# Kernel tuning notes

Measured on AMD Instinct MI355X. Metric: run time of the kernel, lower is better.

## Reference

```python
import jax, jax.numpy as jnp
import numpy as np

N = 5000      # nodes
E = 80000     # edges (avg degree 16)
B = 8         # batch of graph signals sharing one graph
IN = 30       # input feature dim (10 steps x 3)
H = 4         # attention heads
D = 64        # hidden dim per head
HD = H * D    # 256
OUT = 3       # output features per step
NUM_GAT_LAYERS = 4  # num_layer=5 -> 1 + (5-2) layers
EPS = 1e-5


def setup_inputs() -> dict:
    key = jax.random.key(0)
    ks = jax.random.split(key, 40)
    inp = {}
    inp["xx"] = jax.random.normal(ks[0], (B, N, IN), dtype=jnp.float32)
    inp["src"] = jax.random.randint(ks[1], (E,), 0, N, dtype=jnp.int32)
    inp["dst"] = jax.random.randint(ks[2], (E,), 0, N, dtype=jnp.int32)
    dims = [IN, HD, HD, HD]
    k = 3
    for l in range(NUM_GAT_LAYERS):
        fan_in = dims[l]
        inp[f"W{l}"] = jax.random.normal(ks[k], (fan_in, HD), dtype=jnp.float32) / np.sqrt(fan_in); k += 1
        inp[f"al{l}"] = jax.random.normal(ks[k], (H, D), dtype=jnp.float32) * 0.1; k += 1
        inp[f"ar{l}"] = jax.random.normal(ks[k], (H, D), dtype=jnp.float32) * 0.1; k += 1
        inp[f"gamma{l}"] = jnp.ones((HD,), dtype=jnp.float32)
        inp[f"beta{l}"] = jnp.zeros((HD,), dtype=jnp.float32)
    inp["W_out"] = jax.random.normal(ks[k], (HD, OUT), dtype=jnp.float32) / np.sqrt(HD); k += 1
    inp["b_out"] = jnp.zeros((OUT,), dtype=jnp.float32)
    inp["output_length"] = 5
    return inp


def _gat_conv(x, W, al, ar, src, dst):
    # DGL GATConv: fc -> per-head attn logits -> edge softmax over dst -> scatter-sum
    h = (x @ W).reshape(N, H, D)                       # [N,H,D]
    el = (h * al).sum(-1)                              # [N,H]
    er = (h * ar).sum(-1)                              # [N,H]
    e = jax.nn.leaky_relu(el[src] + er[dst], 0.2)      # [E,H]
    m = jax.ops.segment_max(e, dst, num_segments=N)    # [N,H] (stable softmax)
    ex = jnp.exp(e - m[dst])                           # [E,H]
    s = jax.ops.segment_sum(ex, dst, num_segments=N)   # [N,H]
    alpha = ex / s[dst]                                # [E,H]
    return jax.ops.segment_sum(alpha[:, :, None] * h[src], dst, num_segments=N)  # [N,H,D]


def _gat_layer(x, W, al, ar, gamma, beta, src, dst):
    # per-sample GATConv, flatten heads, BatchNorm1d (training stats) over (B,N), LeakyReLU
    out = jax.vmap(lambda xb: _gat_conv(xb, W, al, ar, src, dst))(x)  # [B,N,H,D]
    out = out.reshape(B, N, HD)
    mu = out.mean(axis=(0, 1))
    var = out.var(axis=(0, 1))  # biased, matches torch BN normalization
    out = (out - mu) * jax.lax.rsqrt(var + EPS) * gamma + beta
    return jax.nn.leaky_relu(out, 0.01)


def reference(xx, src, dst,
              W0, al0, ar0, gamma0, beta0,
              W1, al1, ar1, gamma1, beta1,
              W2, al2, ar2, gamma2, beta2,
              W3, al3, ar3, gamma3, beta3,
              W_out, b_out, output_length):
    layers = [(W0, al0, ar0, gamma0, beta0),
              (W1, al1, ar1, gamma1, beta1),
              (W2, al2, ar2, gamma2, beta2),
              (W3, al3, ar3, gamma3, beta3)]
    outputs = []
    for _ in range(output_length):
        h = xx
        for (W, al, ar, g, b) in layers:
            h = _gat_layer(h, W, al, ar, g, b, src, dst)
        out = h @ W_out + b_out                      # [B,N,OUT]
        xx = jnp.concatenate([xx[:, :, 3:], out], axis=-1)
        outputs.append(out[:, :, None, :])
    return jnp.concatenate(outputs, axis=2)          # [B,N,T,OUT]
```

## Files before the change

### kernel.cpp

```cpp
#include <hip/hip_runtime.h>
#include <math.h>

#define NNODES 5000
#define NEDGES 80000
#define NB 8
#define NIN 30
#define K0PAD 32
#define NH 4
#define ND 64
#define NHD 256
#define NT 5
#define NOUT 3
#define ROWS (NB * NNODES)
#define BNEPS 1e-5f
#define KP 40
#define NREP 64
#define BM 32

#define GLOBAL_AS __attribute__((address_space(1)))
#define LDS_AS __attribute__((address_space(3)))

typedef short shortx8 __attribute__((ext_vector_type(8)));
typedef _Float16 halfx8 __attribute__((ext_vector_type(8)));
typedef _Float16 halfx4 __attribute__((ext_vector_type(4)));
typedef _Float16 halfx2 __attribute__((ext_vector_type(2)));
typedef float floatx4 __attribute__((ext_vector_type(4)));

static __device__ __forceinline__ unsigned short f2h(float f) {
    union { _Float16 h; unsigned short u; } v;
    v.h = (_Float16)f;
    return v.u;
}
static __device__ __forceinline__ float h2f(unsigned short u) {
    union { _Float16 h; unsigned short u; } v;
    v.u = u;
    return (float)v.h;
}


__global__ void count_kernel(const int* __restrict__ dst, int* __restrict__ counts, int n) {
    int e = blockIdx.x * blockDim.x + threadIdx.x;
    if (e < n) atomicAdd(&counts[dst[e]], 1);
}

__global__ __launch_bounds__(1024) void scan_kernel(const int* __restrict__ counts,
                                                    int* __restrict__ offsets, int n) {
    __shared__ int smem[1024];
    const int CH = 5;
    int tid = threadIdx.x;
    int base = tid * CH;
    int loc[CH];
    int s = 0;
    for (int j = 0; j < CH; ++j) {
        int i = base + j;
        int v = (i < n) ? counts[i] : 0;
        loc[j] = s;
        s += v;
    }
    smem[tid] = s;
    __syncthreads();
    for (int off = 1; off < 1024; off <<= 1) {
        int v = (tid >= off) ? smem[tid - off] : 0;
        __syncthreads();
        smem[tid] += v;
        __syncthreads();
    }
    int excl = smem[tid] - s;
    for (int j = 0; j < CH; ++j) {
        int i = base + j;
        if (i < n) offsets[i] = excl + loc[j];
    }
    if (tid == 1023) offsets[n] = smem[1023];
}

__global__ void fill_kernel(const int* __restrict__ src, const int* __restrict__ dst,
                            const int* __restrict__ offsets, int* __restrict__ cursor,
                            int* __restrict__ csr_src, int n) {
    int e = blockIdx.x * blockDim.x + threadIdx.x;
    if (e >= n) return;
    int d = dst[e];
    int pos = offsets[d] + atomicAdd(&cursor[d], 1);
    csr_src[pos] = src[e];
}


__global__ void pack_xx_kernel(const float* __restrict__ xx, unsigned short* __restrict__ xx16) {
    int idx = blockIdx.x * blockDim.x + threadIdx.x;
    if (idx >= ROWS * K0PAD) return;
    int g = idx >> 5;
    int k = idx & 31;
    float v = (k < NIN) ? xx[(size_t)g * NIN + k] : 0.0f;
    xx16[idx] = f2h(v);
}

__global__ void packWt_kernel(const float* __restrict__ W0, const float* __restrict__ W1,
                              const float* __restrict__ W2, const float* __restrict__ W3,
                              unsigned short* __restrict__ P0, unsigned short* __restrict__ P1,
                              unsigned short* __restrict__ P2, unsigned short* __restrict__ P3) {
    int l = blockIdx.y;
    const float* W = (l == 0) ? W0 : (l == 1) ? W1 : (l == 2) ? W2 : W3;
    unsigned short* WtP = (l == 0) ? P0 : (l == 1) ? P1 : (l == 2) ? P2 : P3;
    int Kin = (l == 0) ? NIN : NHD;
    int Kpad = (l == 0) ? K0PAD : NHD;
    int n = blockIdx.x;
    int k = threadIdx.x;
    if (k < Kpad) {
        float v = (k < Kin) ? W[(size_t)k * NHD + n] : 0.0f;
        int t = k >> 5;
        int quad = (k >> 3) & 3;
        int j = k & 7;
        int p = n * 4 + (quad ^ ((n >> 1) & 3));
        WtP[(size_t)t * (NHD * 32) + p * 8 + j] = f2h(v);
    }
}


__global__ __launch_bounds__(256) void bnfinal_kernel(float* __restrict__ sums,
                                                      const float* __restrict__ gamma,
                                                      const float* __restrict__ beta,
                                                      float* __restrict__ bnss) {
    int c = threadIdx.x;
    float s = 0.0f, s2 = 0.0f;
#pragma unroll
    for (int r = 0; r < NREP; ++r) {
        s += sums[r * 2 * NHD + c];
        s2 += sums[r * 2 * NHD + NHD + c];
        sums[r * 2 * NHD + c] = 0.0f;
        sums[r * 2 * NHD + NHD + c] = 0.0f;
    }
    const float invn = 1.0f / (float)ROWS;
    float mu = s * invn;
    float var = s2 * invn - mu * mu;
    float sc = rsqrtf(var + BNEPS) * gamma[c];
    bnss[c] = sc;
    bnss[NHD + c] = beta[c] - mu * sc;
}


__global__ __launch_bounds__(256) void gemm_mfma_kernel(
    const unsigned short* __restrict__ A, const unsigned short* __restrict__ Wt,
    const float* __restrict__ alw, const float* __restrict__ arw,
    const float* __restrict__ bnss, int apply_bn,
    unsigned short* __restrict__ C16, float* __restrict__ el, float* __restrict__ er,
    int K) {
    __shared__ __align__(16) short As[BM * KP];
    __shared__ __align__(16) short Bs[256 * 32];
    __shared__ float bn_scale[NHD];
    __shared__ float bn_shift[NHD];
    int tid = threadIdx.x;
    if (apply_bn) {
        bn_scale[tid] = bnss[tid];
        bn_shift[tid] = bnss[NHD + tid];
    }
    __syncthreads();

    int wave = tid >> 6;
    int lane = tid & 63;
    int c = lane & 15;
    int quad = lane >> 4;
    int xorv = (c >> 1) & 3;
    int row0 = blockIdx.x * BM;

    floatx4 acc[2][4];
#pragma unroll
    for (int mt = 0; mt < 2; ++mt)
#pragma unroll
        for (int nt = 0; nt < 4; ++nt) acc[mt][nt] = (floatx4){0.f, 0.f, 0.f, 0.f};

    int r = tid >> 2;
    int seg = tid & 3;
    for (int k0 = 0; k0 < K; k0 += 32) {
        const unsigned short* gB = Wt + (size_t)(k0 >> 5) * (NHD * 32);
#pragma unroll
        for (int i = 0; i < 4; ++i) {
            int ci = i * 256 + tid;
            __builtin_amdgcn_global_load_lds(
                (const GLOBAL_AS unsigned int*)(gB + ci * 8),
                (LDS_AS unsigned int*)(&Bs[ci * 8]), 16, 0, 0);
        }
        if (r < BM) {
            shortx8 v = *(const shortx8*)(A + (size_t)(row0 + r) * K + k0 + seg * 8);
            if (apply_bn) {
                halfx8 hv = *(halfx8*)&v;
                int kg = k0 + seg * 8;
#pragma unroll
                for (int j = 0; j < 8; ++j) {
                    float x = (float)hv[j];
                    x = fmaf(x, bn_scale[kg + j], bn_shift[kg + j]);
                    x = (x > 0.0f) ? x : 0.01f * x;
                    hv[j] = (_Float16)x;
                }
                v = *(shortx8*)&hv;
            }
            *(shortx8*)(&As[r * KP + seg * 8]) = v;
        }
        __syncthreads();
        halfx8 a[2], b[4];
#pragma unroll
        for (int mt = 0; mt < 2; ++mt)
            a[mt] = *(const halfx8*)(&As[(mt * 16 + c) * KP + quad * 8]);
#pragma unroll
        for (int nt = 0; nt < 4; ++nt) {
            int pq = (wave * 64 + nt * 16 + c) * 4 + (quad ^ xorv);
            b[nt] = *(const halfx8*)(&Bs[pq * 8]);
        }
#pragma unroll
        for (int mt = 0; mt < 2; ++mt)
#pragma unroll
            for (int nt = 0; nt < 4; ++nt)
                acc[mt][nt] = __builtin_amdgcn_mfma_f32_16x16x32_f16(a[mt], b[nt],
                                                                     acc[mt][nt], 0, 0, 0);
        __syncthreads();
    }

    float alv[4], arv[4];
#pragma unroll
    for (int nt = 0; nt < 4; ++nt) {
        alv[nt] = alw[wave * 64 + nt * 16 + c];
        arv[nt] = arw[wave * 64 + nt * 16 + c];
    }
#pragma unroll
    for (int mt = 0; mt < 2; ++mt) {
#pragma unroll
        for (int rr = 0; rr < 4; ++rr) {
            int row = row0 + mt * 16 + quad * 4 + rr;
            float pl = 0.0f, pr = 0.0f;
#pragma unroll
            for (int nt = 0; nt < 4; ++nt) {
                float v = acc[mt][nt][rr];
                C16[(size_t)row * NHD + wave * 64 + nt * 16 + c] = f2h(v);
                pl += v * alv[nt];
                pr += v * arv[nt];
            }
#pragma unroll
            for (int o = 1; o < 16; o <<= 1) {
                pl += __shfl_xor(pl, o);
                pr += __shfl_xor(pr, o);
            }
            if (c == mt * 4 + rr) {
                el[(size_t)row * NH + wave] = pl;
                er[(size_t)row * NH + wave] = pr;
            }
        }
    }
}


__global__ __launch_bounds__(256) void attn_kernel(const unsigned short* __restrict__ h16,
                                                   const float* __restrict__ el,
                                                   const float* __restrict__ er,
                                                   const int* __restrict__ offsets,
                                                   const int* __restrict__ csr_src,
                                                   unsigned short* __restrict__ out16,
                                                   float* __restrict__ sums_cur) {
    __shared__ float bnpart[4][2][NHD];
    int p = blockIdx.x;
    int tid = threadIdx.x;
    int b = p & 7;
    int wave = tid >> 6;
    int lane = tid & 63;
    int head = lane >> 4;
    int li = lane & 15;
    int n = ((p >> 3) << 2) + wave;
    int g = b * NNODES + n;
    int start = offsets[n];
    int deg = offsets[n + 1] - start;
    const float* elb = el + (size_t)b * NNODES * NH;
    float er_nh = er[(size_t)g * NH + head];
    float* bw = &bnpart[wave][0][0];

    if (deg == 0) {
        *(unsigned long long*)(out16 + (size_t)g * NHD + lane * 4) = 0ULL;
        int c4 = lane * 4;
#pragma unroll
        for (int j = 0; j < 4; ++j) {
            bw[c4 + j] = 0.0f;
            bw[NHD + c4 + j] = 0.0f;
        }
    } else if (deg <= 64) {
        float e[4], w[4];
        int s[4];
#pragma unroll
        for (int k = 0; k < 4; ++k) {
            int idx = k * 16 + li;
            if (idx < deg) {
                s[k] = csr_src[start + idx];
                float t = elb[s[k] * NH + head] + er_nh;
                e[k] = (t > 0.0f) ? t : 0.2f * t;
            } else {
                s[k] = 0;
                e[k] = -INFINITY;
            }
        }
        float mx = fmaxf(fmaxf(e[0], e[1]), fmaxf(e[2], e[3]));
#pragma unroll
        for (int o = 8; o; o >>= 1) mx = fmaxf(mx, __shfl_xor(mx, o));
        float sm = 0.0f;
#pragma unroll
        for (int k = 0; k < 4; ++k) {
            w[k] = __expf(e[k] - mx);
            sm += w[k];
        }
#pragma unroll
        for (int o = 8; o; o >>= 1) sm += __shfl_xor(sm, o);

        int sub = lane >> 5;
        int i32 = lane & 31;
        int hsel = (lane & 24) << 1;
        float smh = __shfl(sm, hsel);
        const unsigned short* hrow = h16 + (size_t)b * NNODES * NHD + i32 * 8;
        float a0 = 0.f, a1 = 0.f, a2 = 0.f, a3 = 0.f;
        float a4 = 0.f, a5 = 0.f, a6 = 0.f, a7 = 0.f;
#define GATHER_CHUNK(K)                                                          \
        if (deg > (K) * 16) {                                                    \
            int cnt = deg - (K) * 16;                                            \
            cnt = (cnt > 16) ? 16 : cnt;                                         \
            int j = 0;                                                           \
            for (; j + 4 <= cnt; j += 4) {                                       \
                int sa = __shfl(s[K], j + sub);                                  \
                float wa = __shfl(w[K], hsel + j + sub);                         \
                int sb = __shfl(s[K], j + 2 + sub);                              \
                float wb = __shfl(w[K], hsel + j + 2 + sub);                     \
                halfx8 ha = *(const halfx8*)(hrow + (size_t)sa * NHD);           \
                halfx8 hb = *(const halfx8*)(hrow + (size_t)sb * NHD);           \
                a0 += wa * (float)ha[0]; a1 += wa * (float)ha[1];                \
                a2 += wa * (float)ha[2]; a3 += wa * (float)ha[3];                \
                a4 += wa * (float)ha[4]; a5 += wa * (float)ha[5];                \
                a6 += wa * (float)ha[6]; a7 += wa * (float)ha[7];                \
                a0 += wb * (float)hb[0]; a1 += wb * (float)hb[1];                \
                a2 += wb * (float)hb[2]; a3 += wb * (float)hb[3];                \
                a4 += wb * (float)hb[4]; a5 += wb * (float)hb[5];                \
                a6 += wb * (float)hb[6]; a7 += wb * (float)hb[7];                \
            }                                                                    \
            for (; j < cnt; j += 2) {                                            \
                int e2 = j + sub;                                                \
                bool valid = (e2 < cnt);                                         \
                int ec = valid ? e2 : (cnt - 1);                                 \
                int sa = __shfl(s[K], ec);                                       \
                float wa0 = __shfl(w[K], hsel + ec);                             \
                float wa = valid ? wa0 : 0.0f;                                   \
                halfx8 ha = *(const halfx8*)(hrow + (size_t)sa * NHD);           \
                a0 += wa * (float)ha[0]; a1 += wa * (float)ha[1];                \
                a2 += wa * (float)ha[2]; a3 += wa * (float)ha[3];                \
                a4 += wa * (float)ha[4]; a5 += wa * (float)ha[5];                \
                a6 += wa * (float)ha[6]; a7 += wa * (float)ha[7];                \
            }                                                                    \
        }
        GATHER_CHUNK(0)
        GATHER_CHUNK(1)
        GATHER_CHUNK(2)
        GATHER_CHUNK(3)
#undef GATHER_CHUNK
        a0 += __shfl_xor(a0, 32); a1 += __shfl_xor(a1, 32);
        a2 += __shfl_xor(a2, 32); a3 += __shfl_xor(a3, 32);
        a4 += __shfl_xor(a4, 32); a5 += __shfl_xor(a5, 32);
        a6 += __shfl_xor(a6, 32); a7 += __shfl_xor(a7, 32);
        if (sub == 0) {
            float inv = 1.0f / smh;
            halfx8 o8;
            o8[0] = (_Float16)(a0 * inv); o8[1] = (_Float16)(a1 * inv);
            o8[2] = (_Float16)(a2 * inv); o8[3] = (_Float16)(a3 * inv);
            o8[4] = (_Float16)(a4 * inv); o8[5] = (_Float16)(a5 * inv);
            o8[6] = (_Float16)(a6 * inv); o8[7] = (_Float16)(a7 * inv);
            *(halfx8*)(out16 + (size_t)g * NHD + i32 * 8) = o8;
            int c8 = i32 * 8;
#pragma unroll
            for (int j = 0; j < 8; ++j) {
                float v = (float)o8[j];
                bw[c8 + j] = v;
                bw[NHD + c8 + j] = v * v;
            }
        }
    } else {
        const unsigned short* hbase = h16 + (size_t)b * NNODES * NHD + lane * 4;
        float mx = -INFINITY;
        for (int i = li; i < deg; i += 16) {
            int s2 = csr_src[start + i];
            float t = elb[s2 * NH + head] + er_nh;
            t = (t > 0.0f) ? t : 0.2f * t;
            mx = fmaxf(mx, t);
        }
#pragma unroll
        for (int o = 8; o; o >>= 1) mx = fmaxf(mx, __shfl_xor(mx, o));
        float sm = 0.0f;
        for (int i = li; i < deg; i += 16) {
            int s2 = csr_src[start + i];
            float t = elb[s2 * NH + head] + er_nh;
            t = (t > 0.0f) ? t : 0.2f * t;
            sm += __expf(t - mx);
        }
#pragma unroll
        for (int o = 8; o; o >>= 1) sm += __shfl_xor(sm, o);
        float a0 = 0.f, a1 = 0.f, a2 = 0.f, a3 = 0.f;
        for (int j = 0; j < deg; ++j) {
            int s2 = csr_src[start + j];
            float t = elb[s2 * NH + head] + er_nh;
            t = (t > 0.0f) ? t : 0.2f * t;
            float wj = __expf(t - mx);
            halfx4 hv = *(const halfx4*)(hbase + (size_t)s2 * NHD);
            a0 += wj * (float)hv[0];
            a1 += wj * (float)hv[1];
            a2 += wj * (float)hv[2];
            a3 += wj * (float)hv[3];
        }
        float inv = 1.0f / sm;
        halfx4 o4;
        o4[0] = (_Float16)(a0 * inv);
        o4[1] = (_Float16)(a1 * inv);
        o4[2] = (_Float16)(a2 * inv);
        o4[3] = (_Float16)(a3 * inv);
        *(halfx4*)(out16 + (size_t)g * NHD + lane * 4) = o4;
        int c4 = lane * 4;
#pragma unroll
        for (int j = 0; j < 4; ++j) {
            float v = (float)o4[j];
            bw[c4 + j] = v;
            bw[NHD + c4 + j] = v * v;
        }
    }
    __syncthreads();
    {
        int c = tid;
        float s = bnpart[0][0][c] + bnpart[1][0][c] + bnpart[2][0][c] + bnpart[3][0][c];
        float s2 = bnpart[0][1][c] + bnpart[1][1][c] + bnpart[2][1][c] + bnpart[3][1][c];
        float* sr = sums_cur + (p & (NREP - 1)) * 2 * NHD;
        atomicAdd(&sr[c], s);
        atomicAdd(&sr[NHD + c], s2);
    }
}


__global__ __launch_bounds__(256) void headout_kernel(const unsigned short* __restrict__ x16,
                                                      const float* __restrict__ bnss,
                                                      const float* __restrict__ Wout,
                                                      const float* __restrict__ bout,
                                                      float* __restrict__ out,
                                                      unsigned short* __restrict__ xx16, int t) {
    __shared__ float bsc[NHD];
    __shared__ float bsh[NHD];
    {
        int c = threadIdx.x;
        bsc[c] = bnss[c];
        bsh[c] = bnss[NHD + c];
    }
    __syncthreads();

    int wave = threadIdx.x >> 6;
    int lane = threadIdx.x & 63;
    int g = blockIdx.x * 4 + wave;
    int c0 = lane * 4;
    halfx4 hv = *(const halfx4*)(x16 + (size_t)g * NHD + c0);
    float vv[4];
#pragma unroll
    for (int j = 0; j < 4; ++j) {
        float x = fmaf((float)hv[j], bsc[c0 + j], bsh[c0 + j]);
        vv[j] = (x > 0.0f) ? x : 0.01f * x;
    }
    float r0 = vv[0] * Wout[(c0 + 0) * NOUT + 0] + vv[1] * Wout[(c0 + 1) * NOUT + 0] +
               vv[2] * Wout[(c0 + 2) * NOUT + 0] + vv[3] * Wout[(c0 + 3) * NOUT + 0];
    float r1 = vv[0] * Wout[(c0 + 0) * NOUT + 1] + vv[1] * Wout[(c0 + 1) * NOUT + 1] +
               vv[2] * Wout[(c0 + 2) * NOUT + 1] + vv[3] * Wout[(c0 + 3) * NOUT + 1];
    float r2 = vv[0] * Wout[(c0 + 0) * NOUT + 2] + vv[1] * Wout[(c0 + 1) * NOUT + 2] +
               vv[2] * Wout[(c0 + 2) * NOUT + 2] + vv[3] * Wout[(c0 + 3) * NOUT + 2];
#pragma unroll
    for (int o = 32; o; o >>= 1) {
        r0 += __shfl_xor(r0, o);
        r1 += __shfl_xor(r1, o);
        r2 += __shfl_xor(r2, o);
    }
    float o0 = r0 + bout[0], o1 = r1 + bout[1], o2 = r2 + bout[2];
    if (lane == 0) {
        float* op = out + ((size_t)g * NT + t) * NOUT;
        op[0] = o0;
        op[1] = o1;
        op[2] = o2;
    }
    float oldv = (lane < NIN) ? h2f(xx16[(size_t)g * K0PAD + lane]) : 0.0f;
    float shifted = __shfl(oldv, lane + 3);
    float newv = (lane < 27) ? shifted : (lane == 27 ? o0 : (lane == 28 ? o1 : o2));
    if (lane < NIN) xx16[(size_t)g * K0PAD + lane] = f2h(newv);
}


extern "C" void kernel_launch(void* const* d_in, const int* in_sizes, int n_in,
                              void* d_out, int out_size, void* d_ws, size_t ws_size,
                              hipStream_t stream) {
    const float* xx = (const float*)d_in[0];
    const int* src = (const int*)d_in[1];
    const int* dst = (const int*)d_in[2];
    const float* W[4] = {(const float*)d_in[3], (const float*)d_in[8],
                         (const float*)d_in[13], (const float*)d_in[18]};
    const float* al[4] = {(const float*)d_in[4], (const float*)d_in[9],
                          (const float*)d_in[14], (const float*)d_in[19]};
    const float* ar[4] = {(const float*)d_in[5], (const float*)d_in[10],
                          (const float*)d_in[15], (const float*)d_in[20]};
    const float* gamma[4] = {(const float*)d_in[6], (const float*)d_in[11],
                             (const float*)d_in[16], (const float*)d_in[21]};
    const float* beta[4] = {(const float*)d_in[7], (const float*)d_in[12],
                            (const float*)d_in[17], (const float*)d_in[22]};
    const float* W_out = (const float*)d_in[23];
    const float* b_out = (const float*)d_in[24];
    float* out = (float*)d_out;

    float* wsf = (float*)d_ws;
    float* el = wsf;
    float* er = el + (size_t)ROWS * NH;
    float* sums = er + (size_t)ROWS * NH;
    float* bnss = sums + NREP * 2 * NHD;
    unsigned short* h16 = (unsigned short*)(bnss + 2 * NHD);
    unsigned short* act16 = h16 + (size_t)ROWS * NHD;
    unsigned short* xx16 = act16 + (size_t)ROWS * NHD;
    unsigned short* Wt0 = xx16 + (size_t)ROWS * K0PAD;
    unsigned short* Wt1 = Wt0 + 256 * K0PAD;
    unsigned short* Wt2 = Wt1 + 256 * NHD;
    unsigned short* Wt3 = Wt2 + 256 * NHD;
    int* counts = (int*)(Wt3 + 256 * NHD);
    int* offsets = counts + NNODES;
    int* cursor = offsets + NNODES + 8;
    int* csr_src = cursor + NNODES;
    const unsigned short* Wt[4] = {Wt0, Wt1, Wt2, Wt3};

    hipMemsetAsync(counts, 0, NNODES * sizeof(int), stream);
    hipMemsetAsync(sums, 0, NREP * 2 * NHD * sizeof(float), stream);
    count_kernel<<<(NEDGES + 255) / 256, 256, 0, stream>>>(dst, counts, NEDGES);
    scan_kernel<<<1, 1024, 0, stream>>>(counts, offsets, NNODES);
    hipMemsetAsync(cursor, 0, NNODES * sizeof(int), stream);
    fill_kernel<<<(NEDGES + 255) / 256, 256, 0, stream>>>(src, dst, offsets, cursor,
                                                          csr_src, NEDGES);
    pack_xx_kernel<<<(ROWS * K0PAD + 255) / 256, 256, 0, stream>>>(xx, xx16);
    packWt_kernel<<<dim3(256, 4), 256, 0, stream>>>(W[0], W[1], W[2], W[3],
                                                    (unsigned short*)Wt0,
                                                    (unsigned short*)Wt1,
                                                    (unsigned short*)Wt2,
                                                    (unsigned short*)Wt3);

    for (int t = 0; t < NT; ++t) {
        for (int l = 0; l < 4; ++l) {
            const unsigned short* A16 = (l == 0) ? xx16 : act16;
            int K = (l == 0) ? K0PAD : NHD;
            int apply_bn = (l > 0) ? 1 : 0;
            gemm_mfma_kernel<<<ROWS / BM, 256, 0, stream>>>(A16, Wt[l], al[l], ar[l],
                                                            bnss, apply_bn,
                                                            h16, el, er, K);
            attn_kernel<<<ROWS / 4, 256, 0, stream>>>(h16, el, er, offsets, csr_src,
                                                      act16, sums);
            bnfinal_kernel<<<1, 256, 0, stream>>>(sums, gamma[l], beta[l], bnss);
        }
        headout_kernel<<<ROWS / 4, 256, 0, stream>>>(act16, bnss, W_out, b_out,
                                                     out, xx16, t);
    }
}
```

Measured before the change: 1.336 ms.

## Use packed fp16 math for BN prologue and attention gather; stage GEMM output in LDS

```diff
diff --git a/kernel.cpp b/kernel.cpp
--- a/kernel.cpp
+++ b/kernel.cpp
@@ -16,6 +16,7 @@
 #define KP 40
 #define NREP 64
 #define BM 32
+#define CSTR 264
 
 #define GLOBAL_AS __attribute__((address_space(1)))
 #define LDS_AS __attribute__((address_space(3)))
@@ -25,6 +26,7 @@
 typedef _Float16 halfx4 __attribute__((ext_vector_type(4)));
 typedef _Float16 halfx2 __attribute__((ext_vector_type(2)));
 typedef float floatx4 __attribute__((ext_vector_type(4)));
+typedef int intx4 __attribute__((ext_vector_type(4)));
 
 static __device__ __forceinline__ unsigned short f2h(float f) {
     union { _Float16 h; unsigned short u; } v;
@@ -35,6 +37,9 @@
     union { _Float16 h; unsigned short u; } v;
     v.u = u;
     return (float)v.h;
+}
+static __device__ __forceinline__ halfx8 splat8(_Float16 x) {
+    return (halfx8){x, x, x, x, x, x, x, x};
 }
 
 
@@ -143,14 +148,15 @@
     const float* __restrict__ bnss, int apply_bn,
     unsigned short* __restrict__ C16, float* __restrict__ el, float* __restrict__ er,
     int K) {
-    __shared__ __align__(16) short As[BM * KP];
-    __shared__ __align__(16) short Bs[256 * 32];
-    __shared__ float bn_scale[NHD];
-    __shared__ float bn_shift[NHD];
+    __shared__ __align__(16) short smem_s[BM * KP + NHD * 32];
+    __shared__ __align__(16) unsigned short bnsc16[NHD];
+    __shared__ __align__(16) unsigned short bnsh16[NHD];
+    short* As = smem_s;
+    short* Bs = smem_s + BM * KP;
     int tid = threadIdx.x;
     if (apply_bn) {
-        bn_scale[tid] = bnss[tid];
-        bn_shift[tid] = bnss[NHD + tid];
+        bnsc16[tid] = f2h(bnss[tid]);
+        bnsh16[tid] = f2h(bnss[NHD + tid]);
     }
     __syncthreads();
 
@@ -169,6 +175,7 @@
 
     int r = tid >> 2;
     int seg = tid & 3;
+    const halfx8 p01 = splat8((_Float16)0.01f);
     for (int k0 = 0; k0 < K; k0 += 32) {
         const unsigned short* gB = Wt + (size_t)(k0 >> 5) * (NHD * 32);
 #pragma unroll
@@ -183,13 +190,10 @@
             if (apply_bn) {
                 halfx8 hv = *(halfx8*)&v;
                 int kg = k0 + seg * 8;
-#pragma unroll
-                for (int j = 0; j < 8; ++j) {
-                    float x = (float)hv[j];
-                    x = fmaf(x, bn_scale[kg + j], bn_shift[kg + j]);
-                    x = (x > 0.0f) ? x : 0.01f * x;
-                    hv[j] = (_Float16)x;
-                }
+                halfx8 sc = *(const halfx8*)(&bnsc16[kg]);
+                halfx8 sh = *(const halfx8*)(&bnsh16[kg]);
+                halfx8 x = hv * sc + sh;
+                hv = __builtin_elementwise_max(x, x * p01);
                 v = *(shortx8*)&hv;
             }
             *(shortx8*)(&As[r * KP + seg * 8]) = v;
@@ -213,6 +217,7 @@
         __syncthreads();
     }
 
+    short* Cs = smem_s;
     float alv[4], arv[4];
 #pragma unroll
     for (int nt = 0; nt < 4; ++nt) {
@@ -223,12 +228,13 @@
     for (int mt = 0; mt < 2; ++mt) {
 #pragma unroll
         for (int rr = 0; rr < 4; ++rr) {
-            int row = row0 + mt * 16 + quad * 4 + rr;
+            int rl = mt * 16 + quad * 4 + rr;
+            int row = row0 + rl;
             float pl = 0.0f, pr = 0.0f;
 #pragma unroll
             for (int nt = 0; nt < 4; ++nt) {
                 float v = acc[mt][nt][rr];
-                C16[(size_t)row * NHD + wave * 64 + nt * 16 + c] = f2h(v);
+                Cs[rl * CSTR + wave * 64 + nt * 16 + c] = (short)f2h(v);
                 pl += v * alv[nt];
                 pr += v * arv[nt];
             }
@@ -242,6 +248,14 @@
                 er[(size_t)row * NH + wave] = pr;
             }
         }
+    }
+    __syncthreads();
+#pragma unroll
+    for (int i = 0; i < 4; ++i) {
+        int rl = i * 8 + (tid >> 5);
+        int col = (tid & 31) * 8;
+        shortx8 vv = *(const shortx8*)(&Cs[rl * CSTR + col]);
+        *(shortx8*)(&C16[(size_t)(row0 + rl) * NHD + col]) = vv;
     }
 }
 
@@ -308,9 +322,9 @@
         int i32 = lane & 31;
         int hsel = (lane & 24) << 1;
         float smh = __shfl(sm, hsel);
+        float invsm = 1.0f / smh;
         const unsigned short* hrow = h16 + (size_t)b * NNODES * NHD + i32 * 8;
-        float a0 = 0.f, a1 = 0.f, a2 = 0.f, a3 = 0.f;
-        float a4 = 0.f, a5 = 0.f, a6 = 0.f, a7 = 0.f;
+        halfx8 acc = splat8((_Float16)0.0f);
 #define GATHER_CHUNK(K)                                                          \
         if (deg > (K) * 16) {                                                    \
             int cnt = deg - (K) * 16;                                            \
@@ -323,14 +337,8 @@
                 float wb = __shfl(w[K], hsel + j + 2 + sub);                     \
                 halfx8 ha = *(const halfx8*)(hrow + (size_t)sa * NHD);           \
                 halfx8 hb = *(const halfx8*)(hrow + (size_t)sb * NHD);           \
-                a0 += wa * (float)ha[0]; a1 += wa * (float)ha[1];                \
-                a2 += wa * (float)ha[2]; a3 += wa * (float)ha[3];                \
-                a4 += wa * (float)ha[4]; a5 += wa * (float)ha[5];                \
-                a6 += wa * (float)ha[6]; a7 += wa * (float)ha[7];                \
-                a0 += wb * (float)hb[0]; a1 += wb * (float)hb[1];                \
-                a2 += wb * (float)hb[2]; a3 += wb * (float)hb[3];                \
-                a4 += wb * (float)hb[4]; a5 += wb * (float)hb[5];                \
-                a6 += wb * (float)hb[6]; a7 += wb * (float)hb[7];                \
+                acc += ha * splat8((_Float16)(wa * invsm));                      \
+                acc += hb * splat8((_Float16)(wb * invsm));                      \
             }                                                                    \
             for (; j < cnt; j += 2) {                                            \
                 int e2 = j + sub;                                                \
@@ -338,12 +346,9 @@
                 int ec = valid ? e2 : (cnt - 1);                                 \
                 int sa = __shfl(s[K], ec);                                       \
                 float wa0 = __shfl(w[K], hsel + ec);                             \
-                float wa = valid ? wa0 : 0.0f;                                   \
+                float wa = valid ? wa0 * invsm : 0.0f;                           \
                 halfx8 ha = *(const halfx8*)(hrow + (size_t)sa * NHD);           \
-                a0 += wa * (float)ha[0]; a1 += wa * (float)ha[1];                \
-                a2 += wa * (float)ha[2]; a3 += wa * (float)ha[3];                \
-                a4 += wa * (float)ha[4]; a5 += wa * (float)ha[5];                \
-                a6 += wa * (float)ha[6]; a7 += wa * (float)ha[7];                \
+                acc += ha * splat8((_Float16)wa);                                \
             }                                                                    \
         }
         GATHER_CHUNK(0)
@@ -351,22 +356,19 @@
         GATHER_CHUNK(2)
         GATHER_CHUNK(3)
 #undef GATHER_CHUNK
-        a0 += __shfl_xor(a0, 32); a1 += __shfl_xor(a1, 32);
-        a2 += __shfl_xor(a2, 32); a3 += __shfl_xor(a3, 32);
-        a4 += __shfl_xor(a4, 32); a5 += __shfl_xor(a5, 32);
-        a6 += __shfl_xor(a6, 32); a7 += __shfl_xor(a7, 32);
+        intx4 ai = *(intx4*)&acc;
+        intx4 bi;
+        bi[0] = __shfl_xor(ai[0], 32);
+        bi[1] = __shfl_xor(ai[1], 32);
+        bi[2] = __shfl_xor(ai[2], 32);
+        bi[3] = __shfl_xor(ai[3], 32);
+        acc += *(halfx8*)&bi;
         if (sub == 0) {
-            float inv = 1.0f / smh;
-            halfx8 o8;
-            o8[0] = (_Float16)(a0 * inv); o8[1] = (_Float16)(a1 * inv);
-            o8[2] = (_Float16)(a2 * inv); o8[3] = (_Float16)(a3 * inv);
-            o8[4] = (_Float16)(a4 * inv); o8[5] = (_Float16)(a5 * inv);
-            o8[6] = (_Float16)(a6 * inv); o8[7] = (_Float16)(a7 * inv);
-            *(halfx8*)(out16 + (size_t)g * NHD + i32 * 8) = o8;
+            *(halfx8*)(out16 + (size_t)g * NHD + i32 * 8) = acc;
             int c8 = i32 * 8;
 #pragma unroll
             for (int j = 0; j < 8; ++j) {
-                float v = (float)o8[j];
+                float v = (float)acc[j];
                 bw[c8 + j] = v;
                 bw[NHD + c8 + j] = v * v;
             }
```

Measured after the change: 1.322 ms. No clear change (-1.1%).
